# Kernel tuning notes

Measured on AMD Instinct MI355X. Metric: run time of the kernel, lower is better.

Reference implementation:

```python
import jax, jax.numpy as jnp
import numpy as np

B, C, L, H = 4, 128, 4096, 4
GROUPS, EPS = 32, 1e-5


def group_norm(x, gamma, beta):
    # x: [B, C, L]; normalize per (batch, group) over (C//G, L)
    b, c, l = x.shape
    xg = x.reshape(b, GROUPS, c // GROUPS, l)
    mu = jnp.mean(xg, axis=(2, 3), keepdims=True)
    var = jnp.var(xg, axis=(2, 3), keepdims=True)
    xn = ((xg - mu) * jax.lax.rsqrt(var + EPS)).reshape(b, c, l)
    return xn * gamma[None, :, None] + beta[None, :, None]


def setup_inputs() -> dict:
    key = jax.random.key(0)
    k1, k2, k3 = jax.random.split(key, 3)
    return {
        "x": jax.random.normal(k1, (B, C, L), dtype=jnp.float32),
        "w_qkv": jax.random.normal(k2, (3 * C, C), dtype=jnp.float32) * 0.02,
        "w_proj": jax.random.normal(k3, (C, C), dtype=jnp.float32) * 0.02,
        "b_proj": jnp.zeros((C,), dtype=jnp.float32),
        "gn_gamma": jnp.ones((C,), dtype=jnp.float32),
        "gn_beta": jnp.zeros((C,), dtype=jnp.float32),
    }


def reference(x, w_qkv, w_proj, b_proj, gn_gamma, gn_beta):
    b, c, l = x.shape
    hd = c // H
    h = group_norm(x, gn_gamma, gn_beta)
    # 1x1 conv == channel matmul: [B, 3C, L]
    qkv = jnp.einsum('oc,bcl->bol', w_qkv, h)
    # torch reshape(B*H, 3C/H, L).chunk(3, dim=1): per-head contiguous slices
    qkv = qkv.reshape(b, H, 3 * hd, l)
    q, k, v = qkv[:, :, :hd], qkv[:, :, hd:2 * hd], qkv[:, :, 2 * hd:]
    scale = 1.0 / np.sqrt(np.sqrt(hd)).astype(np.float32)
    attn = jnp.einsum('bhct,bhcs->bhts', q * scale, k * scale)
    attn = jax.nn.softmax(attn, axis=-1)
    o = jnp.einsum('bhts,bhcs->bhct', attn, v).reshape(b, c, l)
    o = jnp.einsum('oc,bcl->bol', w_proj, o) + b_proj[None, :, None]
    return o + x
```

## Files before the change

### kernel.cpp

```cpp
#include <hip/hip_runtime.h>
#include <hip/hip_bf16.h>
#include <cstdint>
#include <cstddef>


#define B_ 4
#define C_ 128
#define L_ 4096
#define H_ 4
#define HD_ 32
#define NG_ 32
#define CPG_ 4
#define EPS_ 1e-5f
#define QKSCALE_ 0.5050097650430367f

typedef __attribute__((ext_vector_type(8))) short bf16x8;
typedef __attribute__((ext_vector_type(8))) unsigned short u16x8;
typedef __attribute__((ext_vector_type(4))) float f32x4;
typedef __attribute__((ext_vector_type(16))) float f32x16;
typedef __attribute__((ext_vector_type(2))) _Float16 f16x2;
typedef __attribute__((ext_vector_type(4))) _Float16 f16x4;
typedef __attribute__((ext_vector_type(8))) _Float16 f16x8;
typedef __attribute__((ext_vector_type(2))) unsigned int u32x2;
typedef __attribute__((ext_vector_type(4))) unsigned int u32x4;

#if __has_builtin(__builtin_amdgcn_exp2f)
#define EXP2F(x) __builtin_amdgcn_exp2f(x)
#else
#define EXP2F(x) exp2f(x)
#endif

__device__ __forceinline__ float bu2f(unsigned short u) {
  return __builtin_bit_cast(float, (unsigned int)(((unsigned int)u) << 16));
}
__device__ __forceinline__ unsigned short f2bu(float f) {
  unsigned int u = __builtin_bit_cast(unsigned int, f);
  unsigned int r = (u + 0x7fffu + ((u >> 16) & 1u)) >> 16;
  return (unsigned short)r;
}
__device__ __forceinline__ float4 u42f4(ushort4 u) {
  return make_float4(bu2f(u.x), bu2f(u.y), bu2f(u.z), bu2f(u.w));
}
__device__ __forceinline__ unsigned int pkbf(float a, float b) {
  return (unsigned int)f2bu(a) | ((unsigned int)f2bu(b) << 16);
}
__device__ __forceinline__ f16x2 pkhf2(float a, float b) {
#if __has_builtin(__builtin_amdgcn_cvt_pkrtz)
  return __builtin_bit_cast(f16x2, __builtin_amdgcn_cvt_pkrtz(a, b));
#else
  f16x2 r;
  r[0] = (_Float16)a;
  r[1] = (_Float16)b;
  return r;
#endif
}
__device__ __forceinline__ unsigned int pkhf(float a, float b) {
  return __builtin_bit_cast(unsigned int, pkhf2(a, b));
}

__device__ __forceinline__ void gload16(const void* g, void* l) {
  __builtin_amdgcn_global_load_lds(
      (const __attribute__((address_space(1))) unsigned int*)g,
      (__attribute__((address_space(3))) unsigned int*)l, 16, 0, 0);
}

__device__ __forceinline__ bool detect_fast(const ushort* x) {
  __shared__ int flag_s;
  int t = threadIdx.x;
  if (t < 64) {
    int e = (x[t] >> 7) & 0xFF;
    unsigned long long m = __ballot((e < 64) || (e > 192));
    if (t == 0) flag_s = (__popcll(m) > 4) ? 1 : 0;
  }
  __syncthreads();
  return flag_s != 0;
}

__device__ __forceinline__ float4 ldx4(const void* x, size_t idx, bool f32) {
  if (f32) return *((const float4*)x + (idx >> 2));
  ushort4 u = *((const ushort4*)x + (idx >> 2));
  return u42f4(u);
}

__global__ __launch_bounds__(256) void gn_stats(const void* __restrict__ x,
                                                const void* __restrict__ wq,
                                                const void* __restrict__ wp,
                                                const void* __restrict__ bp,
                                                ushort* __restrict__ wq_b,
                                                ushort* __restrict__ wp_b,
                                                float* __restrict__ bp_f,
                                                float2* __restrict__ gpart) {
  bool f32 = detect_fast((const ushort*)x);
  int blk = blockIdx.x;
  int t = threadIdx.x;

  if (blk >= 256) {
    int i0 = ((blk - 256) * 256 + t) * 8;
#pragma unroll
    for (int k = 0; k < 8; ++k) {
      int i = i0 + k;
      if (i >= 65664) break;
      if (i < 49152) {
        wq_b[i] = f32 ? f2bu(((const float*)wq)[i]) : ((const ushort*)wq)[i];
      } else if (i < 65536) {
        int off = i - 49152;
        wp_b[off] = f32 ? f2bu(((const float*)wp)[off]) : ((const ushort*)wp)[off];
      } else {
        int off = i - 65536;
        bp_f[off] = f32 ? ((const float*)bp)[off] : bu2f(((const ushort*)bp)[off]);
      }
    }
    return;
  }

  int b = blk >> 6, rem = blk & 63;
  int g = rem >> 1, half = rem & 1;
  size_t base = ((size_t)b * C_ + (size_t)g * CPG_) * L_ + (size_t)half * 2048;

  float s = 0.f, ss = 0.f;
#pragma unroll
  for (int cc = 0; cc < 4; ++cc) {
#pragma unroll
    for (int i = 0; i < 2; ++i) {
      size_t e = base + (size_t)cc * L_ + i * 1024 + t * 4;
      float4 f = ldx4(x, e, f32);
      s += f.x + f.y + f.z + f.w;
      ss += f.x * f.x + f.y * f.y + f.z * f.z + f.w * f.w;
    }
  }
#pragma unroll
  for (int m = 32; m >= 1; m >>= 1) {
    s += __shfl_xor(s, m, 64);
    ss += __shfl_xor(ss, m, 64);
  }
  __shared__ float red[4][2];
  int wv = t >> 6;
  if ((t & 63) == 0) { red[wv][0] = s; red[wv][1] = ss; }
  __syncthreads();
  if (t == 0) {
    float ts = red[0][0] + red[1][0] + red[2][0] + red[3][0];
    float tss = red[0][1] + red[1][1] + red[2][1] + red[3][1];
    gpart[(b * 32 + g) * 2 + half] = make_float2(ts, tss);
  }
}

__global__ __launch_bounds__(256) void qkv_kernel(const ushort* __restrict__ wq_b,
                                                  const void* __restrict__ x,
                                                  const float2* __restrict__ gpart,
                                                  const void* __restrict__ gm,
                                                  const void* __restrict__ bt,
                                                  ushort* __restrict__ Qt,
                                                  ushort* __restrict__ Kt,
                                                  ushort* __restrict__ Vb) {
  bool f32 = detect_fast((const ushort*)x);
  __shared__ alignas(16) ushort Hs[64][136];
  __shared__ alignas(16) float Ls[64][69];
  __shared__ float2 abs_s[128];

  int lx = blockIdx.x, oz = blockIdx.y, b = blockIdx.z;
  int t = threadIdx.x;
  int w = t >> 6, lane = t & 63, l16 = lane & 15, q = lane >> 4, q8 = q * 8;

  if (t < 64) {
#pragma unroll
    for (int k = 0; k < 2; ++k) {
      int c = 2 * t + k;
      int g = c >> 2;
      float2 p0 = gpart[(b * 32 + g) * 2];
      float2 p1 = gpart[(b * 32 + g) * 2 + 1];
      float mu = (p0.x + p1.x) * (1.0f / 16384.0f);
      float var = (p0.y + p1.y) * (1.0f / 16384.0f) - mu * mu;
      float rs = rsqrtf(var + EPS_);
      float ga = f32 ? ((const float*)gm)[c] : bu2f(((const ushort*)gm)[c]);
      float be = f32 ? ((const float*)bt)[c] : bu2f(((const ushort*)bt)[c]);
      abs_s[c] = make_float2(ga * rs, be - mu * ga * rs);
    }
  }
  __syncthreads();

  {
    int u = t & 63, lh = (t >> 6) * 16;
    int c0 = 2 * u;
    float2 ab0 = abs_s[c0];
    float2 ab1 = abs_s[c0 + 1];
    size_t xo = ((size_t)b * C_ + c0) * L_ + (size_t)lx * 64 + lh;
#pragma unroll
    for (int j = 0; j < 4; ++j) {
      float4 f0 = ldx4(x, xo + j * 4, f32);
      float4 f1 = ldx4(x, xo + L_ + j * 4, f32);
      float n0[4] = {f0.x * ab0.x + ab0.y, f0.y * ab0.x + ab0.y,
                     f0.z * ab0.x + ab0.y, f0.w * ab0.x + ab0.y};
      float n1[4] = {f1.x * ab1.x + ab1.y, f1.y * ab1.x + ab1.y,
                     f1.z * ab1.x + ab1.y, f1.w * ab1.x + ab1.y};
#pragma unroll
      for (int k = 0; k < 4; ++k)
        *(unsigned int*)&Hs[lh + j * 4 + k][c0] = pkbf(n0[k], n1[k]);
    }
  }
  __syncthreads();

  for (int j = 0; j < 2; ++j) {
    int oy = oz * 2 + j;
    const ushort* wg = wq_b + (size_t)(oy * 64 + w * 16 + l16) * C_;

    f32x4 acc[4] = {{0.f, 0.f, 0.f, 0.f}, {0.f, 0.f, 0.f, 0.f},
                    {0.f, 0.f, 0.f, 0.f}, {0.f, 0.f, 0.f, 0.f}};
#pragma unroll
    for (int kc = 0; kc < 4; ++kc) {
      bf16x8 aw = *(const bf16x8*)(wg + kc * 32 + q8);
#pragma unroll
      for (int nb = 0; nb < 4; ++nb) {
        bf16x8 bh = *(const bf16x8*)&Hs[nb * 16 + l16][kc * 32 + q8];
        acc[nb] = __builtin_amdgcn_mfma_f32_16x16x32_bf16(aw, bh, acc[nb], 0, 0, 0);
      }
    }
    __syncthreads();
#pragma unroll
    for (int nb = 0; nb < 4; ++nb)
#pragma unroll
      for (int r = 0; r < 4; ++r)
        Ls[nb * 16 + l16][w * 16 + 4 * q + r] = acc[nb][r];
    __syncthreads();

#pragma unroll
    for (int hhalf = 0; hhalf < 2; ++hhalf) {
      int hh = oy * 2 + hhalf;
      int type = hh % 3, head = hh / 3;
      size_t bh = (size_t)b * H_ + head;
      if (type == 2) {
        int c_loc = t >> 3, l8 = (t & 7) * 8;
        float v[8];
#pragma unroll
        for (int jj = 0; jj < 8; ++jj) v[jj] = Ls[l8 + jj][hhalf * 32 + c_loc];
        uint4 u;
        u.x = pkhf(v[0], v[1]);
        u.y = pkhf(v[2], v[3]);
        u.z = pkhf(v[4], v[5]);
        u.w = pkhf(v[6], v[7]);
        *(uint4*)(Vb + (bh * 32 + c_loc) * L_ + (size_t)lx * 64 + l8) = u;
      } else {
        ushort* dst = type ? Kt : Qt;
        int l = t >> 2, seg = (t & 3) * 8;
        const float* src = &Ls[l][hhalf * 32 + seg];
        uint4 u;
        u.x = pkbf(src[0] * QKSCALE_, src[1] * QKSCALE_);
        u.y = pkbf(src[2] * QKSCALE_, src[3] * QKSCALE_);
        u.z = pkbf(src[4] * QKSCALE_, src[5] * QKSCALE_);
        u.w = pkbf(src[6] * QKSCALE_, src[7] * QKSCALE_);
        *(uint4*)(dst + ((bh * L_) + lx * 64 + l) * 32 + seg) = u;
      }
    }
  }
}

__global__ __launch_bounds__(512, 8) void attn_kernel(const ushort* __restrict__ Qt,
                                                      const ushort* __restrict__ Kt,
                                                      const ushort* __restrict__ Vb,
                                                      float* __restrict__ Po,
                                                      float* __restrict__ Lg) {
  __shared__ alignas(16) char smem[35840];

  int t = threadIdx.x;
  int w = t >> 6, lane = t & 63, l31 = lane & 31, hi = lane >> 5;
  int qt = w & 3, sh = w >> 2;
  int tq0 = blockIdx.x * 128;
  int ss = blockIdx.y;
  int bh = blockIdx.z;
  int b = bh >> 2, head = bh & 3;
  const ushort* Qg = Qt + ((size_t)bh * L_ + tq0) * 32;
  const ushort* Kg = Kt + ((size_t)bh * L_ + (size_t)ss * 2048) * 32;
  const ushort* Vg = Vb + (size_t)bh * 32 * L_ + (size_t)ss * 2048;

  int rd = t >> 2, pd = t & 3;
  int kcsem = (pd - rd) & 3;
  const ushort* ksrc = Kg + (size_t)rd * 32 + kcsem * 8;
  int vr = t >> 4, vp = t & 15;
  int vcsem = (vp & 8) | ((vp & 7) ^ (vr & 7));
  const ushort* vsrc = Vg + (size_t)vr * L_ + vcsem * 8;

  char* kb0 = smem;
  char* kb1 = smem + 8192;
  char* vb0 = smem + 16384;
  char* vb1 = smem + 24576;

  const ushort* qbase = Qg + (size_t)(qt * 32 + l31) * 32;
  bf16x8 qB0 = *(const bf16x8*)(qbase + 8 * hi);
  bf16x8 qB1 = *(const bf16x8*)(qbase + 16 + 8 * hi);

  const f16x2 one2 = {(_Float16)1.0f, (_Float16)1.0f};

  gload16(ksrc, kb0 + (size_t)t * 16);
  gload16(vsrc, vb0 + (size_t)t * 16);
  ksrc += 4096;
  vsrc += 128;
  __syncthreads();

  f32x16 aO = {0.f};
  float lsum = 0.f;

  int flip = 0;
  for (int it = 0; it < 16; ++it) {
    if (it < 15) {
      gload16(ksrc, (flip ? kb0 : kb1) + (size_t)t * 16);
      gload16(vsrc, (flip ? vb0 : vb1) + (size_t)t * 16);
      ksrc += 4096;
      vsrc += 128;
    }
    const ushort* kc = (const ushort*)(flip ? kb1 : kb0);
    const ushort* vc = (const ushort*)(flip ? vb1 : vb0);

#pragma unroll
    for (int st = 0; st < 2; ++st) {
      int s0 = 64 * sh + 32 * st;
      const ushort* krow = kc + (size_t)(s0 + l31) * 32;
      bf16x8 aK0 = *(const bf16x8*)(krow + ((hi + l31) & 3) * 8);
      bf16x8 aK1 = *(const bf16x8*)(krow + ((2 + hi + l31) & 3) * 8);
      f32x16 zz = {0.f};
      f32x16 sf;
      __builtin_amdgcn_s_setprio(1);
      sf = __builtin_amdgcn_mfma_f32_32x32x16_bf16(aK0, qB0, zz, 0, 0, 0);
      sf = __builtin_amdgcn_mfma_f32_32x32x16_bf16(aK1, qB1, sf, 0, 0, 0);
      __builtin_amdgcn_s_setprio(0);

#pragma unroll
      for (int sb = 0; sb < 2; ++sb) {
        int sblk = 4 * sh + 2 * st + sb;
        int kci = 2 * sblk + hi;
        int vpos = (kci & 8) | ((kci & 7) ^ (l31 & 7));
        f16x8 vf = *(const f16x8*)(vc + (size_t)l31 * 128 + vpos * 8);

        float p0 = EXP2F(sf[8 * sb + 0]);
        float p1 = EXP2F(sf[8 * sb + 1]);
        float p2 = EXP2F(sf[8 * sb + 2]);
        float p3 = EXP2F(sf[8 * sb + 3]);
        float p4 = EXP2F(sf[8 * sb + 4]);
        float p5 = EXP2F(sf[8 * sb + 5]);
        float p6 = EXP2F(sf[8 * sb + 6]);
        float p7 = EXP2F(sf[8 * sb + 7]);
        f16x2 cA0 = pkhf2(p0, p1), cA1 = pkhf2(p2, p3);
        f16x2 cB0 = pkhf2(p4, p5), cB1 = pkhf2(p6, p7);
        lsum = __builtin_amdgcn_fdot2(cA0, one2, lsum, false);
        lsum = __builtin_amdgcn_fdot2(cA1, one2, lsum, false);
        lsum = __builtin_amdgcn_fdot2(cB0, one2, lsum, false);
        lsum = __builtin_amdgcn_fdot2(cB1, one2, lsum, false);

        u32x2 r0 = __builtin_amdgcn_permlane32_swap(
            __builtin_bit_cast(unsigned int, cA0),
            __builtin_bit_cast(unsigned int, cB0), false, false);
        u32x2 r1 = __builtin_amdgcn_permlane32_swap(
            __builtin_bit_cast(unsigned int, cA1),
            __builtin_bit_cast(unsigned int, cB1), false, false);
        u32x4 pw = {r0.x, r1.x, r0.y, r1.y};
        f16x8 pf = __builtin_bit_cast(f16x8, pw);

        __builtin_amdgcn_s_setprio(1);
        aO = __builtin_amdgcn_mfma_f32_32x32x16_f16(vf, pf, aO, 0, 0, 0);
        __builtin_amdgcn_s_setprio(0);
      }
    }
    __syncthreads();
    flip ^= 1;
  }

  float* Osh = (float*)smem;
  float* Lp = (float*)(smem + 33792);
  {
    float* ob = Osh + (size_t)(sh * 4 + qt) * (32 * 33) + (size_t)l31 * 33;
#pragma unroll
    for (int reg = 0; reg < 16; ++reg) {
      int R = (reg & 3) + 8 * (reg >> 2) + 4 * hi;
      ob[R] = aO[reg];
    }
    Lp[(sh * 2 + hi) * 128 + qt * 32 + l31] = lsum;
  }
  __syncthreads();

  {
    int qloc = t >> 2, c0 = (t & 3) * 8;
    int qt2 = qloc >> 5, q31 = qloc & 31;
    float lt = Lp[qloc] + Lp[128 + qloc] + Lp[256 + qloc] + Lp[384 + qloc];
    const float* o0 = Osh + (size_t)qt2 * (32 * 33) + (size_t)q31 * 33 + c0;
    const float* o1 = o0 + 4 * (32 * 33);
    float o[8];
#pragma unroll
    for (int jj = 0; jj < 8; ++jj) o[jj] = o0[jj] + o1[jj];
    float* dst = Po + (size_t)ss * ((size_t)B_ * L_ * C_) +
                 ((size_t)b * L_ + tq0 + qloc) * C_ + head * 32 + c0;
    *(float4*)dst = make_float4(o[0], o[1], o[2], o[3]);
    *(float4*)(dst + 4) = make_float4(o[4], o[5], o[6], o[7]);
    if ((t & 3) == 0) Lg[((size_t)ss * 16 + bh) * L_ + tq0 + qloc] = lt;
  }
}

__global__ __launch_bounds__(256) void combine_kernel(const float* __restrict__ Po,
                                                      const float* __restrict__ Lg,
                                                      ushort* __restrict__ ot) {
  int tl = blockIdx.x * 256 + threadIdx.x;
  int row = tl >> 4;
  int c0 = (tl & 15) * 8;
  int head = c0 >> 5;
  int b = row >> 12, l = row & 4095;
  const size_t HALF = (size_t)B_ * L_ * C_;
  const float* p0 = Po + (size_t)row * C_ + c0;
  const float* p1 = p0 + HALF;
  float lv = Lg[(size_t)(b * 4 + head) * L_ + l] +
             Lg[(size_t)(16 + b * 4 + head) * L_ + l];
  float inv = 1.0f / lv;
  float4 a0 = *(const float4*)p0;
  float4 a1 = *(const float4*)(p0 + 4);
  float4 b0 = *(const float4*)p1;
  float4 b1 = *(const float4*)(p1 + 4);
  uint4 u;
  u.x = pkbf((a0.x + b0.x) * inv, (a0.y + b0.y) * inv);
  u.y = pkbf((a0.z + b0.z) * inv, (a0.w + b0.w) * inv);
  u.z = pkbf((a1.x + b1.x) * inv, (a1.y + b1.y) * inv);
  u.w = pkbf((a1.z + b1.z) * inv, (a1.w + b1.w) * inv);
  *(uint4*)(ot + (size_t)row * C_ + c0) = u;
}

__global__ __launch_bounds__(256) void proj_kernel(const ushort* __restrict__ wp_b,
                                                   const float* __restrict__ bias,
                                                   const void* __restrict__ x,
                                                   const ushort* __restrict__ ot,
                                                   void* __restrict__ out) {
  bool f32 = detect_fast((const ushort*)x);
  __shared__ alignas(16) float Ls[64][37];

  int lx = blockIdx.x, oy = blockIdx.y, b = blockIdx.z;
  int t = threadIdx.x;
  int w = t >> 6, lane = t & 63, l16 = lane & 15, q = lane >> 4, q8 = q * 8;

  const ushort* wg = wp_b + (size_t)(oy * 64 + w * 16 + l16) * C_;
  const ushort* og = ot + ((size_t)b * L_ + (size_t)lx * 32) * C_;

  f32x4 acc[2] = {{0.f, 0.f, 0.f, 0.f}, {0.f, 0.f, 0.f, 0.f}};
#pragma unroll
  for (int kc = 0; kc < 4; ++kc) {
    bf16x8 aw = *(const bf16x8*)(wg + kc * 32 + q8);
#pragma unroll
    for (int nb = 0; nb < 2; ++nb) {
      bf16x8 bo = *(const bf16x8*)(og + (size_t)(nb * 16 + l16) * C_ + kc * 32 + q8);
      acc[nb] = __builtin_amdgcn_mfma_f32_16x16x32_bf16(aw, bo, acc[nb], 0, 0, 0);
    }
  }
#pragma unroll
  for (int nb = 0; nb < 2; ++nb)
#pragma unroll
    for (int r = 0; r < 4; ++r)
      Ls[w * 16 + 4 * q + r][nb * 16 + l16] = acc[nb][r];
  __syncthreads();

  {
    int o_loc = t >> 2, ls0 = (t & 3) * 8;
    float bv = bias[oy * 64 + o_loc];
    size_t off = ((size_t)b * C_ + oy * 64 + o_loc) * L_ + (size_t)lx * 32 + ls0;
#pragma unroll
    for (int jj = 0; jj < 2; ++jj) {
      float4 xf = ldx4(x, off + jj * 4, f32);
      const float* sp = &Ls[o_loc][ls0 + jj * 4];
      float4 r = make_float4(sp[0] + bv + xf.x, sp[1] + bv + xf.y,
                             sp[2] + bv + xf.z, sp[3] + bv + xf.w);
      if (f32) {
        *(float4*)((float*)out + off + jj * 4) = r;
      } else {
        *(ushort4*)((ushort*)out + off + jj * 4) =
            make_ushort4(f2bu(r.x), f2bu(r.y), f2bu(r.z), f2bu(r.w));
      }
    }
  }
}

extern "C" void kernel_launch(void* const* d_in, const int* in_sizes, int n_in,
                              void* d_out, int out_size, void* d_ws, size_t ws_size,
                              hipStream_t stream) {
  const void* x      = d_in[0];
  const void* w_qkv  = d_in[1];
  const void* w_proj = d_in[2];
  const void* b_proj = d_in[3];
  const void* gamma  = d_in[4];
  const void* beta   = d_in[5];

  char* wsb = (char*)d_ws;
  ushort* wq_b  = (ushort*)(wsb + 0);
  ushort* wp_b  = (ushort*)(wsb + 98304);
  float*  bp_f  = (float*)(wsb + 131072);
  float2* gpart = (float2*)(wsb + 131584);
  float*  Lg    = (float*)(wsb + 139264);
  ushort* Qt    = (ushort*)(wsb + 8388608);
  ushort* ot    = (ushort*)(wsb + 8388608);
  ushort* Kt    = (ushort*)(wsb + 12582912);
  ushort* Vb    = (ushort*)(wsb + 16777216);
  float*  Po    = (float*)(wsb + 20971520);

  gn_stats<<<dim3(289), dim3(256), 0, stream>>>(x, w_qkv, w_proj, b_proj,
                                                wq_b, wp_b, bp_f, gpart);
  qkv_kernel<<<dim3(L_ / 64, 3, B_), dim3(256), 0, stream>>>(wq_b, x, gpart, gamma, beta,
                                                             Qt, Kt, Vb);
  attn_kernel<<<dim3(L_ / 128, 2, B_ * H_), dim3(512), 0, stream>>>(Qt, Kt, Vb, Po, Lg);
  combine_kernel<<<dim3(1024), dim3(256), 0, stream>>>(Po, Lg, ot);
  proj_kernel<<<dim3(L_ / 32, C_ / 64, B_), dim3(256), 0, stream>>>(wp_b, bp_f, x, ot, d_out);
}
```

Before: 146.6 us.

## Remove split-K attention, fuse combine, use 4-stage K/V pipeline

Attention no longer splits the key sequence across two blocks. Each block now walks all 4096 keys and normalizes and writes the bf16 output directly, so the combine kernel and the fp32 partial-output round trip through memory are gone. The K/V double buffer becomes a 4-slot ring with 3 tiles in flight, using explicit vmcnt waits and a single barrier per iteration in place of two syncthreads. The trade-off is half as many blocks (512 instead of 1024), 64KB of LDS per block, which cuts occupancy, and a serial loop twice as long per block.

```diff
diff --git a/kernel.cpp b/kernel.cpp
--- a/kernel.cpp
+++ b/kernel.cpp
@@ -253,23 +253,21 @@
   }
 }
 
-__global__ __launch_bounds__(512, 8) void attn_kernel(const ushort* __restrict__ Qt,
-                                                      const ushort* __restrict__ Kt,
-                                                      const ushort* __restrict__ Vb,
-                                                      float* __restrict__ Po,
-                                                      float* __restrict__ Lg) {
-  __shared__ alignas(16) char smem[35840];
+__global__ __launch_bounds__(512) void attn_kernel(const ushort* __restrict__ Qt,
+                                                   const ushort* __restrict__ Kt,
+                                                   const ushort* __restrict__ Vb,
+                                                   ushort* __restrict__ ot) {
+  __shared__ alignas(16) char smem[65536];
 
   int t = threadIdx.x;
   int w = t >> 6, lane = t & 63, l31 = lane & 31, hi = lane >> 5;
   int qt = w & 3, sh = w >> 2;
   int tq0 = blockIdx.x * 128;
-  int ss = blockIdx.y;
-  int bh = blockIdx.z;
+  int bh = blockIdx.y;
   int b = bh >> 2, head = bh & 3;
   const ushort* Qg = Qt + ((size_t)bh * L_ + tq0) * 32;
-  const ushort* Kg = Kt + ((size_t)bh * L_ + (size_t)ss * 2048) * 32;
-  const ushort* Vg = Vb + (size_t)bh * 32 * L_ + (size_t)ss * 2048;
+  const ushort* Kg = Kt + (size_t)bh * L_ * 32;
+  const ushort* Vg = Vb + (size_t)bh * 32 * L_;
 
   int rd = t >> 2, pd = t & 3;
   int kcsem = (pd - rd) & 3;
@@ -278,36 +276,47 @@
   int vcsem = (vp & 8) | ((vp & 7) ^ (vr & 7));
   const ushort* vsrc = Vg + (size_t)vr * L_ + vcsem * 8;
 
-  char* kb0 = smem;
-  char* kb1 = smem + 8192;
-  char* vb0 = smem + 16384;
-  char* vb1 = smem + 24576;
-
   const ushort* qbase = Qg + (size_t)(qt * 32 + l31) * 32;
   bf16x8 qB0 = *(const bf16x8*)(qbase + 8 * hi);
   bf16x8 qB1 = *(const bf16x8*)(qbase + 16 + 8 * hi);
 
   const f16x2 one2 = {(_Float16)1.0f, (_Float16)1.0f};
 
-  gload16(ksrc, kb0 + (size_t)t * 16);
-  gload16(vsrc, vb0 + (size_t)t * 16);
-  ksrc += 4096;
-  vsrc += 128;
-  __syncthreads();
+#pragma unroll
+  for (int s = 0; s < 3; ++s) {
+    gload16(ksrc, smem + s * 8192 + (size_t)t * 16);
+    gload16(vsrc, smem + 32768 + s * 8192 + (size_t)t * 16);
+    ksrc += 4096;
+    vsrc += 128;
+  }
 
   f32x16 aO = {0.f};
   float lsum = 0.f;
 
-  int flip = 0;
-  for (int it = 0; it < 16; ++it) {
-    if (it < 15) {
-      gload16(ksrc, (flip ? kb0 : kb1) + (size_t)t * 16);
-      gload16(vsrc, (flip ? vb0 : vb1) + (size_t)t * 16);
+  for (int it = 0; it < 32; ++it) {
+    int rem = 31 - it;
+    if (rem >= 2) {
+      asm volatile("s_waitcnt vmcnt(4)" ::: "memory");
+    } else if (rem == 1) {
+      asm volatile("s_waitcnt vmcnt(2)" ::: "memory");
+    } else {
+      asm volatile("s_waitcnt vmcnt(0)" ::: "memory");
+    }
+    __builtin_amdgcn_sched_barrier(0);
+    __builtin_amdgcn_s_barrier();
+    __builtin_amdgcn_sched_barrier(0);
+
+    if (it < 29) {
+      char* kd = smem + ((it + 3) & 3) * 8192;
+      char* vd = smem + 32768 + ((it + 3) & 3) * 8192;
+      gload16(ksrc, kd + (size_t)t * 16);
+      gload16(vsrc, vd + (size_t)t * 16);
       ksrc += 4096;
       vsrc += 128;
     }
-    const ushort* kc = (const ushort*)(flip ? kb1 : kb0);
-    const ushort* vc = (const ushort*)(flip ? vb1 : vb0);
+
+    const ushort* kc = (const ushort*)(smem + (it & 3) * 8192);
+    const ushort* vc = (const ushort*)(smem + 32768 + (it & 3) * 8192);
 
 #pragma unroll
     for (int st = 0; st < 2; ++st) {
@@ -358,9 +367,8 @@
         __builtin_amdgcn_s_setprio(0);
       }
     }
-    __syncthreads();
-    flip ^= 1;
-  }
+  }
+  __syncthreads();
 
   float* Osh = (float*)smem;
   float* Lp = (float*)(smem + 33792);
@@ -379,43 +387,19 @@
     int qloc = t >> 2, c0 = (t & 3) * 8;
     int qt2 = qloc >> 5, q31 = qloc & 31;
     float lt = Lp[qloc] + Lp[128 + qloc] + Lp[256 + qloc] + Lp[384 + qloc];
+    float inv = 1.0f / lt;
     const float* o0 = Osh + (size_t)qt2 * (32 * 33) + (size_t)q31 * 33 + c0;
     const float* o1 = o0 + 4 * (32 * 33);
     float o[8];
 #pragma unroll
-    for (int jj = 0; jj < 8; ++jj) o[jj] = o0[jj] + o1[jj];
-    float* dst = Po + (size_t)ss * ((size_t)B_ * L_ * C_) +
-                 ((size_t)b * L_ + tq0 + qloc) * C_ + head * 32 + c0;
-    *(float4*)dst = make_float4(o[0], o[1], o[2], o[3]);
-    *(float4*)(dst + 4) = make_float4(o[4], o[5], o[6], o[7]);
-    if ((t & 3) == 0) Lg[((size_t)ss * 16 + bh) * L_ + tq0 + qloc] = lt;
-  }
-}
-
-__global__ __launch_bounds__(256) void combine_kernel(const float* __restrict__ Po,
-                                                      const float* __restrict__ Lg,
-                                                      ushort* __restrict__ ot) {
-  int tl = blockIdx.x * 256 + threadIdx.x;
-  int row = tl >> 4;
-  int c0 = (tl & 15) * 8;
-  int head = c0 >> 5;
-  int b = row >> 12, l = row & 4095;
-  const size_t HALF = (size_t)B_ * L_ * C_;
-  const float* p0 = Po + (size_t)row * C_ + c0;
-  const float* p1 = p0 + HALF;
-  float lv = Lg[(size_t)(b * 4 + head) * L_ + l] +
-             Lg[(size_t)(16 + b * 4 + head) * L_ + l];
-  float inv = 1.0f / lv;
-  float4 a0 = *(const float4*)p0;
-  float4 a1 = *(const float4*)(p0 + 4);
-  float4 b0 = *(const float4*)p1;
-  float4 b1 = *(const float4*)(p1 + 4);
-  uint4 u;
-  u.x = pkbf((a0.x + b0.x) * inv, (a0.y + b0.y) * inv);
-  u.y = pkbf((a0.z + b0.z) * inv, (a0.w + b0.w) * inv);
-  u.z = pkbf((a1.x + b1.x) * inv, (a1.y + b1.y) * inv);
-  u.w = pkbf((a1.z + b1.z) * inv, (a1.w + b1.w) * inv);
-  *(uint4*)(ot + (size_t)row * C_ + c0) = u;
+    for (int jj = 0; jj < 8; ++jj) o[jj] = (o0[jj] + o1[jj]) * inv;
+    uint4 u;
+    u.x = pkbf(o[0], o[1]);
+    u.y = pkbf(o[2], o[3]);
+    u.z = pkbf(o[4], o[5]);
+    u.w = pkbf(o[6], o[7]);
+    *(uint4*)(ot + ((size_t)b * L_ + tq0 + qloc) * C_ + head * 32 + c0) = u;
+  }
 }
 
 __global__ __launch_bounds__(256) void proj_kernel(const ushort* __restrict__ wp_b,
@@ -485,18 +469,15 @@
   ushort* wp_b  = (ushort*)(wsb + 98304);
   float*  bp_f  = (float*)(wsb + 131072);
   float2* gpart = (float2*)(wsb + 131584);
-  float*  Lg    = (float*)(wsb + 139264);
   ushort* Qt    = (ushort*)(wsb + 8388608);
-  ushort* ot    = (ushort*)(wsb + 8388608);
   ushort* Kt    = (ushort*)(wsb + 12582912);
   ushort* Vb    = (ushort*)(wsb + 16777216);
-  float*  Po    = (float*)(wsb + 20971520);
+  ushort* ot    = (ushort*)(wsb + 20971520);
 
   gn_stats<<<dim3(289), dim3(256), 0, stream>>>(x, w_qkv, w_proj, b_proj,
                                                 wq_b, wp_b, bp_f, gpart);
   qkv_kernel<<<dim3(L_ / 64, 3, B_), dim3(256), 0, stream>>>(wq_b, x, gpart, gamma, beta,
                                                              Qt, Kt, Vb);
-  attn_kernel<<<dim3(L_ / 128, 2, B_ * H_), dim3(512), 0, stream>>>(Qt, Kt, Vb, Po, Lg);
-  combine_kernel<<<dim3(1024), dim3(256), 0, stream>>>(Po, Lg, ot);
+  attn_kernel<<<dim3(L_ / 128, B_ * H_), dim3(512), 0, stream>>>(Qt, Kt, Vb, ot);
   proj_kernel<<<dim3(L_ / 32, C_ / 64, B_), dim3(256), 0, stream>>>(wp_b, bp_f, x, ot, d_out);
 }
```

After: 140.5 us. 4.2% less time.
